# Performance work log

Hardware: AMD Instinct MI355X
Metric: run time of the kernel (lower is better)

Reference implementation:

```python
import jax, jax.numpy as jnp
import numpy as np

BETA = 0.9          # snn.Leaky default-ish decay given in module
THRESH = 1.0        # snntorch default threshold


def spike(x):
    # heaviside(x); surrogate grad handled in bwd module
    return (x > 0).astype(x.dtype)


def setup_inputs() -> dict:
    key = jax.random.key(0)
    ks = jax.random.split(key, 5)
    T, B, NI, NH, NO = 100, 512, 784, 1024, 10
    x = jax.random.normal(ks[0], (T, B, NI), dtype=jnp.float32)
    W1 = jax.random.normal(ks[1], (NH, NI), dtype=jnp.float32) / np.sqrt(NI)
    b1 = jax.random.normal(ks[2], (NH,), dtype=jnp.float32) * 0.01
    W2 = jax.random.normal(ks[3], (NO, NH), dtype=jnp.float32) / np.sqrt(NH)
    b2 = jax.random.normal(ks[4], (NO,), dtype=jnp.float32) * 0.01
    return {"x": x, "W1": W1, "b1": b1, "W2": W2, "b2": b2}


def reference(x, W1, b1, W2, b2):
    # x: [T, B, num_inputs]
    B = x.shape[1]
    NH = W1.shape[0]
    NO = W2.shape[0]
    dt = x.dtype

    def step(carry, xt):
        mem1, mem2 = carry
        cur1 = xt @ W1.T + b1                       # [B, NH]
        reset1 = (mem1 > THRESH).astype(dt)         # from previous mem
        mem1 = BETA * mem1 + cur1 - reset1 * THRESH
        spk1 = spike(mem1 - THRESH)
        cur2 = spk1 @ W2.T + b2                     # [B, NO]
        reset2 = (mem2 > THRESH).astype(dt)
        mem2 = BETA * mem2 + cur2 - reset2 * THRESH
        spk2 = spike(mem2 - THRESH)
        return (mem1, mem2), spk2

    init = (jnp.zeros((B, NH), dt), jnp.zeros((B, NO), dt))
    (_, mem2), spk2_rec = jax.lax.scan(step, init, x)
    return spk2_rec, mem2
```

## Files before the change

### kernel.cpp

```cpp
#include <hip/hip_runtime.h>
#include <hip/hip_bf16.h>

#define NI 784
#define NH 1024
#define NO 10
#define BATCH 512
#define TSTEPS 100

#define BM 128
#define BN 128
#define BK 16
#define LDT 132

typedef __attribute__((ext_vector_type(4))) float floatx4;

__global__ __launch_bounds__(256) void init_ws_kernel(float* __restrict__ p, int n) {
  int i = blockIdx.x * 256 + threadIdx.x;
  if (i < n) p[i] = 0.0f;
}

__global__ __launch_bounds__(256) void sgemm1_kernel(
    const float* __restrict__ X,
    const float* __restrict__ W1,
    const float* __restrict__ b1,
    float* __restrict__ C)
{
  __shared__ __align__(16) float As[BK * LDT];
  __shared__ __align__(16) float Bs[BK * LDT];

  const int tid = threadIdx.x;
  const int tx = tid & 15;
  const int ty = tid >> 4;
  const int n0 = blockIdx.x * BN;
  const int m0 = blockIdx.y * BM;

  const int srow  = tid >> 2;
  const int skcol = (tid & 3) * 4;

  float acc[8][8];
#pragma unroll
  for (int i = 0; i < 8; ++i)
#pragma unroll
    for (int j = 0; j < 8; ++j) acc[i][j] = 0.0f;

  const float* Xs  = X  + (size_t)m0 * NI + skcol;
  const float* W1s = W1 + (size_t)n0 * NI + skcol;

  floatx4 xa0 = *(const floatx4*)&Xs [(size_t)(srow)      * NI];
  floatx4 xa1 = *(const floatx4*)&Xs [(size_t)(64 + srow) * NI];
  floatx4 wq0 = *(const floatx4*)&W1s[(size_t)(srow)      * NI];
  floatx4 wq1 = *(const floatx4*)&W1s[(size_t)(64 + srow) * NI];

  for (int kt = 0; kt < NI / BK; ++kt) {
    __syncthreads();
#pragma unroll
    for (int e = 0; e < 4; ++e) {
      As[(skcol + e) * LDT + srow]      = xa0[e];
      As[(skcol + e) * LDT + 64 + srow] = xa1[e];
      Bs[(skcol + e) * LDT + srow]      = wq0[e];
      Bs[(skcol + e) * LDT + 64 + srow] = wq1[e];
    }
    __syncthreads();

    if (kt + 1 < NI / BK) {
      const int k0 = (kt + 1) * BK;
      xa0 = *(const floatx4*)&Xs [(size_t)(srow)      * NI + k0];
      xa1 = *(const floatx4*)&Xs [(size_t)(64 + srow) * NI + k0];
      wq0 = *(const floatx4*)&W1s[(size_t)(srow)      * NI + k0];
      wq1 = *(const floatx4*)&W1s[(size_t)(64 + srow) * NI + k0];
    }

#pragma unroll
    for (int k = 0; k < BK; ++k) {
      const floatx4 av0 = *(const floatx4*)&As[k * LDT + ty * 8];
      const floatx4 av1 = *(const floatx4*)&As[k * LDT + ty * 8 + 4];
      const floatx4 bv0 = *(const floatx4*)&Bs[k * LDT + tx * 4];
      const floatx4 bv1 = *(const floatx4*)&Bs[k * LDT + 64 + tx * 4];
      const float a[8] = {av0[0], av0[1], av0[2], av0[3],
                          av1[0], av1[1], av1[2], av1[3]};
#pragma unroll
      for (int i = 0; i < 8; ++i)
#pragma unroll
        for (int j = 0; j < 4; ++j) {
          acc[i][j]     = fmaf(a[i], bv0[j], acc[i][j]);
          acc[i][4 + j] = fmaf(a[i], bv1[j], acc[i][4 + j]);
        }
    }
  }

#pragma unroll
  for (int i = 0; i < 8; ++i) {
    const int m = m0 + ty * 8 + i;
    floatx4 v0, v1;
#pragma unroll
    for (int j = 0; j < 4; ++j) {
      v0[j] = acc[i][j]     + b1[n0 + tx * 4 + j];
      v1[j] = acc[i][4 + j] + b1[n0 + 64 + tx * 4 + j];
    }
    *(floatx4*)&C[(size_t)m * NH + n0 + tx * 4]      = v0;
    *(floatx4*)&C[(size_t)m * NH + n0 + 64 + tx * 4] = v1;
  }
}

__global__ __launch_bounds__(256) void recur_kernel(
    const float* __restrict__ cur1,
    const float* __restrict__ W2,
    const float* __restrict__ b2,
    float* __restrict__ mem1s,
    float* __restrict__ mem2s,
    float* __restrict__ out,
    long long out_size, int t0, int tc, int last)
{
  const int b    = blockIdx.x;
  const int tid  = threadIdx.x;
  const int lane = tid & 63;
  const int wave = tid >> 6;

  __shared__ float red[4][NO];

  float w[4][NO];
#pragma unroll
  for (int j = 0; j < 4; ++j)
#pragma unroll
    for (int o = 0; o < NO; ++o)
      w[j][o] = W2[o * NH + tid * 4 + j];

  floatx4 m1 = *(const floatx4*)&mem1s[(size_t)b * NH + tid * 4];
  float m2 = 0.0f, bb = 0.0f;
  if (tid < NO) {
    m2 = mem2s[b * NO + tid];
    bb = b2[tid];
  }

  const floatx4* c4 = (const floatx4*)cur1;
  floatx4 c = c4[((size_t)0 * BATCH + b) * (NH / 4) + tid];

  for (int t = 0; t < tc; ++t) {
    floatx4 cn = {0.f, 0.f, 0.f, 0.f};
    if (t + 1 < tc) cn = c4[((size_t)(t + 1) * BATCH + b) * (NH / 4) + tid];

    float a[NO];
#pragma unroll
    for (int o = 0; o < NO; ++o) a[o] = 0.0f;

#pragma unroll
    for (int j = 0; j < 4; ++j) {
      float mj = m1[j];
      float reset = (mj > 1.0f) ? 1.0f : 0.0f;
      mj = 0.9f * mj + c[j] - reset;
      m1[j] = mj;
      float s = (mj > 1.0f) ? 1.0f : 0.0f;
#pragma unroll
      for (int o = 0; o < NO; ++o) a[o] = fmaf(s, w[j][o], a[o]);
    }

#pragma unroll
    for (int m = 1; m <= 32; m <<= 1)
#pragma unroll
      for (int o = 0; o < NO; ++o) a[o] += __shfl_xor(a[o], m, 64);

    if (lane == 0) {
#pragma unroll
      for (int o = 0; o < NO; ++o) red[wave][o] = a[o];
    }
    __syncthreads();

    if (tid < NO) {
      float cur2 = red[0][tid] + red[1][tid] + red[2][tid] + red[3][tid] + bb;
      float reset2 = (m2 > 1.0f) ? 1.0f : 0.0f;
      m2 = 0.9f * m2 + cur2 - reset2;
      float spk2 = (m2 > 1.0f) ? 1.0f : 0.0f;
      long long idx = ((long long)(t0 + t) * BATCH + b) * NO + tid;
      if (idx < out_size) out[idx] = spk2;
    }
    __syncthreads();
    c = cn;
  }

  *(floatx4*)&mem1s[(size_t)b * NH + tid * 4] = m1;
  if (tid < NO) {
    mem2s[b * NO + tid] = m2;
    if (last) {
      long long idx = (long long)TSTEPS * BATCH * NO + b * NO + tid;
      if (idx < out_size) out[idx] = m2;
    }
  }
}

__global__ __launch_bounds__(256) void fused_fp32_kernel(
    const float* __restrict__ x,
    const float* __restrict__ W1,
    const float* __restrict__ b1,
    const float* __restrict__ W2,
    const float* __restrict__ b2,
    float* __restrict__ out, long long out_size)
{
  const int b    = blockIdx.x;
  const int tid  = threadIdx.x;
  const int lane = tid & 63;
  const int wave = tid >> 6;

  __shared__ __align__(16) float xs[NI + 4];
  __shared__ float red[4][NO];

  float w[4][NO];
#pragma unroll
  for (int j = 0; j < 4; ++j)
#pragma unroll
    for (int o = 0; o < NO; ++o)
      w[j][o] = W2[o * NH + tid * 4 + j];

  float bias1[4];
#pragma unroll
  for (int j = 0; j < 4; ++j) bias1[j] = b1[tid * 4 + j];

  float m1[4] = {0.f, 0.f, 0.f, 0.f};
  float m2 = 0.0f, bb = 0.0f;
  if (tid < NO) bb = b2[tid];

  for (int t = 0; t < TSTEPS; ++t) {
    if (tid < 196)
      *(floatx4*)&xs[tid * 4] = *(const floatx4*)&x[((size_t)t * BATCH + b) * NI + tid * 4];
    __syncthreads();

    float a[NO];
#pragma unroll
    for (int o = 0; o < NO; ++o) a[o] = 0.0f;

#pragma unroll
    for (int j = 0; j < 4; ++j) {
      const float* wr = W1 + (size_t)(tid * 4 + j) * NI;
      float dot = 0.0f;
      for (int cch = 0; cch < 196; ++cch) {
        floatx4 wv = *(const floatx4*)&wr[cch * 4];
        floatx4 xv = *(const floatx4*)&xs[cch * 4];
#pragma unroll
        for (int e = 0; e < 4; ++e) dot = fmaf(wv[e], xv[e], dot);
      }
      float cur = dot + bias1[j];
      float mj = m1[j];
      float reset = (mj > 1.0f) ? 1.0f : 0.0f;
      mj = 0.9f * mj + cur - reset;
      m1[j] = mj;
      float s = (mj > 1.0f) ? 1.0f : 0.0f;
#pragma unroll
      for (int o = 0; o < NO; ++o) a[o] = fmaf(s, w[j][o], a[o]);
    }

#pragma unroll
    for (int m = 1; m <= 32; m <<= 1)
#pragma unroll
      for (int o = 0; o < NO; ++o) a[o] += __shfl_xor(a[o], m, 64);

    if (lane == 0) {
#pragma unroll
      for (int o = 0; o < NO; ++o) red[wave][o] = a[o];
    }
    __syncthreads();

    if (tid < NO) {
      float cur2 = red[0][tid] + red[1][tid] + red[2][tid] + red[3][tid] + bb;
      float reset2 = (m2 > 1.0f) ? 1.0f : 0.0f;
      m2 = 0.9f * m2 + cur2 - reset2;
      float spk2 = (m2 > 1.0f) ? 1.0f : 0.0f;
      long long idx = ((long long)t * BATCH + b) * NO + tid;
      if (idx < out_size) out[idx] = spk2;
    }
    __syncthreads();
  }

  if (tid < NO) {
    long long idx = (long long)TSTEPS * BATCH * NO + b * NO + tid;
    if (idx < out_size) out[idx] = m2;
  }
}

extern "C" void kernel_launch(void* const* d_in, const int* in_sizes, int n_in,
                              void* d_out, int out_size, void* d_ws, size_t ws_size,
                              hipStream_t stream) {
  const float* x  = (const float*)d_in[0];
  const float* W1 = (const float*)d_in[1];
  const float* b1 = (const float*)d_in[2];
  const float* W2 = (const float*)d_in[3];
  const float* b2 = (const float*)d_in[4];
  float* out = (float*)d_out;

  const size_t mem1_bytes = (size_t)BATCH * NH * 4;
  const size_t mem2_bytes = (size_t)BATCH * NO * 4;
  size_t fixed = (mem1_bytes + mem2_bytes + 255) & ~(size_t)255;
  const size_t per_step = (size_t)BATCH * NH * 4;

  if (d_ws == nullptr || ws_size < fixed + per_step) {
    fused_fp32_kernel<<<BATCH, 256, 0, stream>>>(x, W1, b1, W2, b2, out,
                                                 (long long)out_size);
    return;
  }

  char* ws = (char*)d_ws;
  float* mem1s = (float*)ws;
  float* mem2s = (float*)(ws + mem1_bytes);
  float* cur1  = (float*)(ws + fixed);

  int Tc = (int)((ws_size - fixed) / per_step);
  if (Tc > TSTEPS) Tc = TSTEPS;

  const int nInit = BATCH * NH + BATCH * NO;
  init_ws_kernel<<<(nInit + 255) / 256, 256, 0, stream>>>((float*)ws, nInit);

  for (int t0 = 0; t0 < TSTEPS; t0 += Tc) {
    const int tc = (TSTEPS - t0 < Tc) ? (TSTEPS - t0) : Tc;
    const int M = tc * BATCH;
    dim3 g(NH / BN, M / BM);
    sgemm1_kernel<<<g, 256, 0, stream>>>(x + (size_t)t0 * BATCH * NI, W1, b1, cur1);
    recur_kernel<<<BATCH, 256, 0, stream>>>(cur1, W2, b2, mem1s, mem2s, out,
                                            (long long)out_size, t0, tc,
                                            (t0 + tc >= TSTEPS) ? 1 : 0);
  }
}
```

Baseline: 1.312 ms.

## Split recurrence into spike-bitmask, parallel cur2, and mem2 scan kernels; double-buffer GEMM

Replaces the per-batch recurrence kernel with three stages. The first scans mem1 per neuron and packs spikes into ballot bitmasks. The second computes cur2 for all timesteps in parallel across batch and time chunks. The third runs the small mem2 scan per output. The SGEMM gains double-buffered LDS with a single barrier per k-step and a block-index swizzle intended to improve cache reuse. This is meant to expose more parallelism than the serial time loop over 512 blocks, but it needs a larger workspace holding all of cur1 plus the bitmasks, and it falls back to the old path when that workspace is unavailable.

```diff
diff --git a/kernel.cpp b/kernel.cpp
--- a/kernel.cpp
+++ b/kernel.cpp
@@ -11,6 +11,7 @@
 #define BN 128
 #define BK 16
 #define LDT 132
+#define TCH 10
 
 typedef __attribute__((ext_vector_type(4))) float floatx4;
 
@@ -25,14 +26,18 @@
     const float* __restrict__ b1,
     float* __restrict__ C)
 {
-  __shared__ __align__(16) float As[BK * LDT];
-  __shared__ __align__(16) float Bs[BK * LDT];
+  __shared__ __align__(16) float As[2][BK * LDT];
+  __shared__ __align__(16) float Bs[2][BK * LDT];
 
   const int tid = threadIdx.x;
   const int tx = tid & 15;
   const int ty = tid >> 4;
-  const int n0 = blockIdx.x * BN;
-  const int m0 = blockIdx.y * BM;
+
+  const int hb    = blockIdx.y * gridDim.x + blockIdx.x;
+  const int chunk = (gridDim.x * gridDim.y) >> 3;
+  const int f     = (hb & 7) * chunk + (hb >> 3);
+  const int n0 = (f & 7) * BN;
+  const int m0 = (f >> 3) * BM;
 
   const int srow  = tid >> 2;
   const int skcol = (tid & 3) * 4;
@@ -51,18 +56,20 @@
   floatx4 wq0 = *(const floatx4*)&W1s[(size_t)(srow)      * NI];
   floatx4 wq1 = *(const floatx4*)&W1s[(size_t)(64 + srow) * NI];
 
-  for (int kt = 0; kt < NI / BK; ++kt) {
-    __syncthreads();
-#pragma unroll
-    for (int e = 0; e < 4; ++e) {
-      As[(skcol + e) * LDT + srow]      = xa0[e];
-      As[(skcol + e) * LDT + 64 + srow] = xa1[e];
-      Bs[(skcol + e) * LDT + srow]      = wq0[e];
-      Bs[(skcol + e) * LDT + 64 + srow] = wq1[e];
-    }
-    __syncthreads();
-
-    if (kt + 1 < NI / BK) {
+#pragma unroll
+  for (int e = 0; e < 4; ++e) {
+    As[0][(skcol + e) * LDT + srow]      = xa0[e];
+    As[0][(skcol + e) * LDT + 64 + srow] = xa1[e];
+    Bs[0][(skcol + e) * LDT + srow]      = wq0[e];
+    Bs[0][(skcol + e) * LDT + 64 + srow] = wq1[e];
+  }
+  __syncthreads();
+
+  const int NKT = NI / BK;
+  for (int kt = 0; kt < NKT; ++kt) {
+    const int cur = kt & 1;
+
+    if (kt + 1 < NKT) {
       const int k0 = (kt + 1) * BK;
       xa0 = *(const floatx4*)&Xs [(size_t)(srow)      * NI + k0];
       xa1 = *(const floatx4*)&Xs [(size_t)(64 + srow) * NI + k0];
@@ -72,10 +79,10 @@
 
 #pragma unroll
     for (int k = 0; k < BK; ++k) {
-      const floatx4 av0 = *(const floatx4*)&As[k * LDT + ty * 8];
-      const floatx4 av1 = *(const floatx4*)&As[k * LDT + ty * 8 + 4];
-      const floatx4 bv0 = *(const floatx4*)&Bs[k * LDT + tx * 4];
-      const floatx4 bv1 = *(const floatx4*)&Bs[k * LDT + 64 + tx * 4];
+      const floatx4 av0 = *(const floatx4*)&As[cur][k * LDT + ty * 8];
+      const floatx4 av1 = *(const floatx4*)&As[cur][k * LDT + ty * 8 + 4];
+      const floatx4 bv0 = *(const floatx4*)&Bs[cur][k * LDT + tx * 4];
+      const floatx4 bv1 = *(const floatx4*)&Bs[cur][k * LDT + 64 + tx * 4];
       const float a[8] = {av0[0], av0[1], av0[2], av0[3],
                           av1[0], av1[1], av1[2], av1[3]};
 #pragma unroll
@@ -86,6 +93,17 @@
           acc[i][4 + j] = fmaf(a[i], bv1[j], acc[i][4 + j]);
         }
     }
+
+    if (kt + 1 < NKT) {
+#pragma unroll
+      for (int e = 0; e < 4; ++e) {
+        As[cur ^ 1][(skcol + e) * LDT + srow]      = xa0[e];
+        As[cur ^ 1][(skcol + e) * LDT + 64 + srow] = xa1[e];
+        Bs[cur ^ 1][(skcol + e) * LDT + srow]      = wq0[e];
+        Bs[cur ^ 1][(skcol + e) * LDT + 64 + srow] = wq1[e];
+      }
+    }
+    __syncthreads();
   }
 
 #pragma unroll
@@ -100,6 +118,142 @@
     *(floatx4*)&C[(size_t)m * NH + n0 + tx * 4]      = v0;
     *(floatx4*)&C[(size_t)m * NH + n0 + 64 + tx * 4] = v1;
   }
+}
+
+__global__ __launch_bounds__(64) void spk1_kernel(
+    const float* __restrict__ cur1,
+    unsigned long long* __restrict__ spk)
+{
+  const int b  = blockIdx.x;
+  const int qq = blockIdx.y;
+  const int l  = threadIdx.x;
+
+  const floatx4* c4 = (const floatx4*)cur1;
+  const size_t stride = (size_t)BATCH * (NH / 4);
+  const size_t base   = (size_t)b * (NH / 4) + qq * 64 + l;
+
+  floatx4 m1 = {0.f, 0.f, 0.f, 0.f};
+  floatx4 c  = c4[base];
+
+  for (int t = 0; t < TSTEPS; ++t) {
+    floatx4 cn = {0.f, 0.f, 0.f, 0.f};
+    if (t + 1 < TSTEPS) cn = c4[base + (size_t)(t + 1) * stride];
+
+    unsigned long long bm0 = 0, bm1 = 0, bm2 = 0, bm3 = 0;
+#pragma unroll
+    for (int j = 0; j < 4; ++j) {
+      float mj = m1[j];
+      float reset = (mj > 1.0f) ? 1.0f : 0.0f;
+      mj = 0.9f * mj + c[j] - reset;
+      m1[j] = mj;
+      unsigned long long bm = __ballot(mj > 1.0f);
+      if (j == 0) bm0 = bm; else if (j == 1) bm1 = bm;
+      else if (j == 2) bm2 = bm; else bm3 = bm;
+    }
+
+    if (l < 4) {
+      unsigned long long v = bm0;
+      if (l == 1) v = bm1;
+      else if (l == 2) v = bm2;
+      else if (l == 3) v = bm3;
+      spk[((size_t)t * BATCH + b) * 16 + qq * 4 + l] = v;
+    }
+    c = cn;
+  }
+}
+
+__global__ __launch_bounds__(256) void cur2_kernel(
+    const unsigned long long* __restrict__ spk,
+    const float* __restrict__ W2,
+    const float* __restrict__ b2,
+    float* __restrict__ cur2T)
+{
+  const int b   = blockIdx.x;
+  const int t0  = blockIdx.y * TCH;
+  const int tid = threadIdx.x;
+  const int lane = tid & 63;
+  const int wave = tid >> 6;
+
+  __shared__ float red[2][4][NO];
+
+  float w[4][NO];
+#pragma unroll
+  for (int j = 0; j < 4; ++j)
+#pragma unroll
+    for (int o = 0; o < NO; ++o)
+      w[j][o] = W2[o * NH + tid * 4 + j];
+
+  float bb = 0.0f;
+  if (tid < NO) bb = b2[tid];
+
+  for (int t = t0; t < t0 + TCH; ++t) {
+    const unsigned long long* pk = spk + ((size_t)t * BATCH + b) * 16 + wave * 4;
+    const unsigned long long p0 = pk[0], p1 = pk[1], p2 = pk[2], p3 = pk[3];
+
+    float a[NO];
+#pragma unroll
+    for (int o = 0; o < NO; ++o) a[o] = 0.0f;
+
+    {
+      const float s0 = (float)((p0 >> lane) & 1ULL);
+#pragma unroll
+      for (int o = 0; o < NO; ++o) a[o] = fmaf(s0, w[0][o], a[o]);
+      const float s1 = (float)((p1 >> lane) & 1ULL);
+#pragma unroll
+      for (int o = 0; o < NO; ++o) a[o] = fmaf(s1, w[1][o], a[o]);
+      const float s2 = (float)((p2 >> lane) & 1ULL);
+#pragma unroll
+      for (int o = 0; o < NO; ++o) a[o] = fmaf(s2, w[2][o], a[o]);
+      const float s3 = (float)((p3 >> lane) & 1ULL);
+#pragma unroll
+      for (int o = 0; o < NO; ++o) a[o] = fmaf(s3, w[3][o], a[o]);
+    }
+
+#pragma unroll
+    for (int m = 1; m <= 32; m <<= 1)
+#pragma unroll
+      for (int o = 0; o < NO; ++o) a[o] += __shfl_xor(a[o], m, 64);
+
+    if (lane == 0) {
+#pragma unroll
+      for (int o = 0; o < NO; ++o) red[t & 1][wave][o] = a[o];
+    }
+    __syncthreads();
+
+    if (tid < NO) {
+      float cur2 = red[t & 1][0][tid] + red[t & 1][1][tid]
+                 + red[t & 1][2][tid] + red[t & 1][3][tid] + bb;
+      cur2T[((size_t)b * NO + tid) * TSTEPS + t] = cur2;
+    }
+  }
+}
+
+__global__ __launch_bounds__(256) void mem2_kernel(
+    const float* __restrict__ cur2T,
+    float* __restrict__ out,
+    long long out_size)
+{
+  const int id = blockIdx.x * 256 + threadIdx.x;
+  if (id >= BATCH * NO) return;
+  const int b = id / NO;
+  const int o = id % NO;
+  const float* row = cur2T + (size_t)id * TSTEPS;
+
+  float m2 = 0.0f;
+#pragma unroll
+  for (int t = 0; t < TSTEPS; t += 4) {
+    const floatx4 v = *(const floatx4*)&row[t];
+#pragma unroll
+    for (int e = 0; e < 4; ++e) {
+      float reset2 = (m2 > 1.0f) ? 1.0f : 0.0f;
+      m2 = 0.9f * m2 + v[e] - reset2;
+      float spk2 = (m2 > 1.0f) ? 1.0f : 0.0f;
+      long long idx = ((long long)(t + e) * BATCH + b) * NO + o;
+      if (idx < out_size) out[idx] = spk2;
+    }
+  }
+  long long idx = (long long)TSTEPS * BATCH * NO + id;
+  if (idx < out_size) out[idx] = m2;
 }
 
 __global__ __launch_bounds__(256) void recur_kernel(
@@ -285,6 +439,28 @@
   const float* b2 = (const float*)d_in[4];
   float* out = (float*)d_out;
 
+  char* ws = (char*)d_ws;
+
+  const size_t cur2T_bytes = (size_t)BATCH * NO * TSTEPS * 4;
+  const size_t head        = (cur2T_bytes + 255) & ~(size_t)255;
+  const size_t cur1_bytes  = (size_t)TSTEPS * BATCH * NH * 4;
+  const size_t pack_bytes  = (size_t)TSTEPS * BATCH * 16 * 8;
+  const size_t need_full   = head + cur1_bytes + pack_bytes;
+
+  if (d_ws != nullptr && ws_size >= need_full) {
+    float* cur2T = (float*)ws;
+    float* cur1  = (float*)(ws + head);
+    unsigned long long* spk = (unsigned long long*)(ws + head + cur1_bytes);
+
+    dim3 g(NH / BN, (TSTEPS * BATCH) / BM);
+    sgemm1_kernel<<<g, 256, 0, stream>>>(x, W1, b1, cur1);
+    spk1_kernel<<<dim3(BATCH, 4), 64, 0, stream>>>(cur1, spk);
+    cur2_kernel<<<dim3(BATCH, TSTEPS / TCH), 256, 0, stream>>>(spk, W2, b2, cur2T);
+    mem2_kernel<<<(BATCH * NO + 255) / 256, 256, 0, stream>>>(cur2T, out,
+                                                              (long long)out_size);
+    return;
+  }
+
   const size_t mem1_bytes = (size_t)BATCH * NH * 4;
   const size_t mem2_bytes = (size_t)BATCH * NO * 4;
   size_t fixed = (mem1_bytes + mem2_bytes + 255) & ~(size_t)255;
@@ -296,7 +472,6 @@
     return;
   }
 
-  char* ws = (char*)d_ws;
   float* mem1s = (float*)ws;
   float* mem2s = (float*)(ws + mem1_bytes);
   float* cur1  = (float*)(ws + fixed);
```

After: 1.777 ms. 35.5% more time.
